# Performance work log

Hardware: AMD Instinct MI355X
Metric: run time of the kernel (lower is better)

Reference implementation:

```python
import jax, jax.numpy as jnp
import numpy as np

N_GRAPHS = 1250
NEG_SLOPE = 0.2

def gat_layer(x, src, dst, W, a_src, a_dst, b, concat):
    # x: [N, Fin]; W: [Fin, H*C]; a_src/a_dst: [H, C]; b: [H*C] or [C]
    N = x.shape[0]
    H, C = a_src.shape
    h = (x @ W).reshape(N, H, C)                      # [N,H,C]
    alpha_s = jnp.sum(h * a_src[None], axis=-1)       # [N,H]
    alpha_d = jnp.sum(h * a_dst[None], axis=-1)       # [N,H]
    e = jax.nn.leaky_relu(alpha_s[src] + alpha_d[dst], NEG_SLOPE)  # [E,H]
    # segment softmax over incoming edges of each target node
    m = jax.ops.segment_max(e, dst, num_segments=N)   # [N,H]
    m = jnp.where(jnp.isfinite(m), m, 0.0)
    ex = jnp.exp(e - m[dst])
    s = jax.ops.segment_sum(ex, dst, num_segments=N)  # [N,H]
    alpha = ex / (s[dst] + 1e-16)                     # [E,H]
    msg = h[src] * alpha[..., None]                   # [E,H,C]
    out = jax.ops.segment_sum(msg, dst, num_segments=N)  # [N,H,C]
    out = out.reshape(N, H * C) if concat else out.mean(axis=1)
    return out + b

def setup_inputs() -> dict:
    key = jax.random.key(0)
    ks = jax.random.split(key, 13)
    N, E = 50000, 100000
    x = jax.random.normal(ks[0], (N, 78), dtype=jnp.float32)
    edge_index = jax.random.randint(ks[1], (2, E), 0, N, dtype=jnp.int64)
    # sorted segment ids -> every graph non-empty (~40 nodes each)
    batch = jnp.sort(jax.random.randint(ks[2], (N,), 0, N_GRAPHS, dtype=jnp.int64))
    g = lambda k, shape, fan: jax.random.normal(k, shape, dtype=jnp.float32) / np.float32(np.sqrt(fan))
    return {
        'x': x, 'edge_index': edge_index, 'batch': batch,
        'W1': g(ks[3], (78, 780), 78), 'a_src1': g(ks[4], (10, 78), 78), 'a_dst1': g(ks[5], (10, 78), 78),
        'b1': jnp.zeros((780,), jnp.float32),
        'W2': g(ks[6], (780, 128), 780), 'a_src2': g(ks[7], (1, 128), 128), 'a_dst2': g(ks[8], (1, 128), 128),
        'b2': jnp.zeros((128,), jnp.float32),
        'fc_w': g(ks[9], (128, 128), 128), 'fc_b': jnp.zeros((128,), jnp.float32),
    }

def reference(x, edge_index, batch, W1, a_src1, a_dst1, b1, W2, a_src2, a_dst2, b2, fc_w, fc_b):
    N = x.shape[0]
    loop = jnp.arange(N, dtype=edge_index.dtype)
    src = jnp.concatenate([edge_index[0], loop])  # add self loops (PyG default)
    dst = jnp.concatenate([edge_index[1], loop])
    # dropout layers are identity in eval mode
    h = jax.nn.elu(gat_layer(x, src, dst, W1, a_src1, a_dst1, b1, concat=True))   # [N,780]
    h = jax.nn.relu(gat_layer(h, src, dst, W2, a_src2, a_dst2, b2, concat=True))  # [N,128]
    g = jax.ops.segment_max(h, batch, num_segments=N_GRAPHS)                      # [G,128]
    g = jnp.where(jnp.isfinite(g), g, 0.0)
    return jax.nn.relu(g @ fc_w + fc_b)
```

## Files before the change

### kernel.cpp

```cpp
#include <hip/hip_runtime.h>
#include <hip/hip_bf16.h>
#include <cstdint>

#define CAP 32
typedef __hip_bfloat16 bf16;
typedef __attribute__((ext_vector_type(8))) short short8;
typedef __attribute__((ext_vector_type(4))) float f32x4;

__device__ __forceinline__ float sb2f(short s) {
  unsigned int u = ((unsigned int)(unsigned short)s) << 16;
  return __uint_as_float(u);
}
__device__ __forceinline__ short f2sb(float f) {
  bf16 h = __float2bfloat16(f);
  return *reinterpret_cast<short*>(&h);
}

__global__ void k_detect(const int* __restrict__ ei, int* __restrict__ flag) {
  __shared__ int any;
  if (threadIdx.x == 0) any = 0;
  __syncthreads();
  int v = 0;
  for (int i = 1 + 2 * threadIdx.x; i < 2000; i += 512) v |= ei[i];
  if (v) atomicOr(&any, 1);
  __syncthreads();
  if (threadIdx.x == 0) flag[0] = (any == 0) ? 1 : 0;
}

__device__ __forceinline__ void edge_sd(const int* __restrict__ ei, int e, int f,
                                        int& src, int& dst) {
  if (e < 100000) {
    if (f) { src = ei[2 * e]; dst = ei[200000 + 2 * e]; }
    else   { src = ei[e];     dst = ei[100000 + e]; }
  } else { src = dst = e - 100000; }
  src = min(max(src, 0), 49999);
  dst = min(max(dst, 0), 49999);
}

__global__ void k_prep(const float* __restrict__ x, const float* __restrict__ W1,
                       const float* __restrict__ W2, const float* __restrict__ aw1,
                       const float* __restrict__ dw1, bf16* __restrict__ xb,
                       bf16* __restrict__ Wat, bf16* __restrict__ W1bdp,
                       bf16* __restrict__ W2h, float* __restrict__ zp, int zeroWords) {
  int i = blockIdx.x * 256 + threadIdx.x;
  if (i < zeroWords) zp[i] = 0.f;
  const int n_xb = 50000 * 96;
  const int n_wa = 32 * 96;
  const int n_bd = 10 * 96 * 96;
  const int n_w2 = 10 * 128 * 96;
  if (i < n_xb) {
    int r = i / 96, k = i - r * 96;
    xb[i] = __float2bfloat16(k < 78 ? x[r * 78 + k] : 0.f);
  } else if (i < n_xb + n_wa) {
    int j = i - n_xb;
    int c = j / 96, k = j - c * 96;
    float s = 0.f;
    if (k < 78 && c < 20) {
      const float* w = (c < 10) ? aw1 : dw1;
      int h = (c < 10) ? c : c - 10;
      const float* wrow = W1 + k * 780 + h * 78;
      const float* arow = w + h * 78;
      for (int q = 0; q < 78; q++) s += wrow[q] * arow[q];
    }
    Wat[c * 96 + k] = __float2bfloat16(s);
  } else if (i < n_xb + n_wa + n_bd) {
    int j = i - n_xb - n_wa;
    int hh = j / 9216;
    int rem = j - hh * 9216;
    int jj = rem / 96, k = rem - jj * 96;
    W1bdp[j] = __float2bfloat16((jj < 78 && k < 78) ? W1[k * 780 + hh * 78 + jj] : 0.f);
  } else if (i < n_xb + n_wa + n_bd + n_w2) {
    int j = i - n_xb - n_wa - n_bd;
    int hh = j / 12288;
    int rem = j - hh * 12288;
    int c = rem / 96, k = rem - c * 96;
    W2h[j] = __float2bfloat16(k < 78 ? W2[(hh * 78 + k) * 128 + c] : 0.f);
  }
}

__global__ __launch_bounds__(256) void k_alpha(const bf16* __restrict__ xb,
                                               const bf16* __restrict__ Wat,
                                               float* __restrict__ as1,
                                               float* __restrict__ ad1) {
  __shared__ __align__(16) short Als[64 * 104];
  __shared__ __align__(16) short Wls[32 * 104];
  const int t = threadIdx.x;
  const int w = t >> 6, l = t & 63, l15 = l & 15, q = l >> 4;
  const int rowBase = blockIdx.x * 64;
  for (int s = t; s < 768; s += 256) {
    int row = s / 12, kg = s - row * 12;
    short8 v = {};
    int gr = rowBase + row;
    if (gr < 50000) v = *(const short8*)((const short*)xb + (size_t)gr * 96 + kg * 8);
    *(short8*)&Als[row * 104 + kg * 8] = v;
  }
  for (int s = t; s < 384; s += 256) {
    int row = s / 12, kg = s - row * 12;
    *(short8*)&Wls[row * 104 + kg * 8] =
        *(const short8*)((const short*)Wat + (size_t)row * 96 + kg * 8);
  }
  __syncthreads();
  f32x4 acc2[2] = {};
#pragma unroll
  for (int ks = 0; ks < 3; ks++) {
    short8 a = *(const short8*)&Als[(w * 16 + l15) * 104 + ks * 32 + q * 8];
#pragma unroll
    for (int nt = 0; nt < 2; nt++) {
      short8 b = *(const short8*)&Wls[(nt * 16 + l15) * 104 + ks * 32 + q * 8];
      acc2[nt] = __builtin_amdgcn_mfma_f32_16x16x32_bf16(a, b, acc2[nt], 0, 0, 0);
    }
  }
  const int gr0 = rowBase + w * 16 + q * 4;
#pragma unroll
  for (int nt = 0; nt < 2; nt++) {
    int c = nt * 16 + l15;
#pragma unroll
    for (int r = 0; r < 4; r++) {
      int gr = gr0 + r;
      if (gr < 50000) {
        if (c < 10)       as1[gr * 10 + c] = acc2[nt][r];
        else if (c < 20)  ad1[gr * 10 + (c - 10)] = acc2[nt][r];
      }
    }
  }
}

__global__ void k_scatter(const int* __restrict__ ei, const int* __restrict__ flag,
                          int* __restrict__ cnt, int* __restrict__ csr) {
  int e = blockIdx.x * 256 + threadIdx.x;
  if (e >= 150000) return;
  int f = flag[0], src, dst;
  edge_sd(ei, e, f, src, dst);
  int pos = atomicAdd(&cnt[dst], 1);
  if (pos < CAP) csr[dst * CAP + pos] = src;
}

__global__ __launch_bounds__(256) void k_aggx(const bf16* __restrict__ xb,
                                              const float* __restrict__ as1,
                                              const float* __restrict__ ad1,
                                              const int* __restrict__ csr,
                                              const int* __restrict__ cnt,
                                              bf16* __restrict__ aggx) {
  __shared__ float sexw[2][CAP * 10];
  __shared__ float sden[2][16];
  __shared__ int ssrc[2][CAP];
  const int t = threadIdx.x;
  const int sub = t >> 7, tt = t & 127;
  const int n = blockIdx.x * 2 + sub;
  if (tt < 16) sden[sub][tt] = 0.f;
  const int cn = min(cnt[n], CAP);
  if (tt < cn) ssrc[sub][tt] = csr[n * CAP + tt];
  __syncthreads();
  for (int wv = tt; wv < cn * 10; wv += 128) {
    int k = wv / 10, h = wv - k * 10;
    int src = ssrc[sub][k];
    float e = as1[src * 10 + h] + ad1[n * 10 + h];
    e = e >= 0.f ? e : 0.2f * e;
    float ex = __expf(e);
    sexw[sub][wv] = ex;
    atomicAdd(&sden[sub][h], ex);
  }
  __syncthreads();
  if (tt < 96) {
    float acc[10];
#pragma unroll
    for (int h = 0; h < 10; h++) acc[h] = 0.f;
    const short* xs = (const short*)xb;
    for (int k = 0; k < cn; k++) {
      int src = ssrc[sub][k];
      float xv = sb2f(xs[(size_t)src * 96 + tt]);
      const float* swk = sexw[sub] + k * 10;
#pragma unroll
      for (int h = 0; h < 10; h++) acc[h] += swk[h] * xv;
    }
    short* outp = (short*)aggx + (size_t)n * 960 + tt;
#pragma unroll
    for (int h = 0; h < 10; h++)
      outp[h * 96] = f2sb(acc[h] / (sden[sub][h] + 1e-16f));
  }
}

__global__ __launch_bounds__(256) void k_gemm2f(const bf16* __restrict__ aggx,
                                                const bf16* __restrict__ W1bdp,
                                                const bf16* __restrict__ W2h,
                                                const float* __restrict__ b1,
                                                const float* __restrict__ AW2,
                                                const float* __restrict__ DW2,
                                                bf16* __restrict__ H2,
                                                float* __restrict__ as2,
                                                float* __restrict__ ad2) {
  __shared__ __align__(16) short Ain[64 * 104];
  __shared__ __align__(16) short Ah[64 * 104];
  __shared__ __align__(16) short Bw[96 * 104];
  __shared__ __align__(16) short Bls[128 * 104];
  __shared__ float sb1[784];
  __shared__ float sS[4][64], sD[4][64];
  const int t = threadIdx.x;
  const int w = t >> 6, l = t & 63, l15 = l & 15, q = l >> 4;
  const int rowBase = blockIdx.x * 64;
  for (int i = t; i < 784; i += 256) sb1[i] = (i < 780) ? b1[i] : 0.f;
  f32x4 acc[4][2] = {};
  for (int h = 0; h < 10; h++) {
    __syncthreads();
#pragma unroll
    for (int i = 0; i < 3; i++) {
      int s = t + i * 256;
      int row = s / 12, kg = s - row * 12;
      int gr = rowBase + row;
      short8 v = {};
      if (gr < 50000)
        v = *(const short8*)((const short*)aggx + ((size_t)gr * 10 + h) * 96 + kg * 8);
      *(short8*)&Ain[row * 104 + kg * 8] = v;
    }
    for (int s = t; s < 1152; s += 256) {
      int row = s / 12, kg = s - row * 12;
      *(short8*)&Bw[row * 104 + kg * 8] =
          *(const short8*)((const short*)W1bdp + (size_t)h * 9216 + row * 96 + kg * 8);
    }
#pragma unroll
    for (int i = 0; i < 6; i++) {
      int s = t + i * 256;
      int col = s / 12, kg = s - col * 12;
      *(short8*)&Bls[col * 104 + kg * 8] =
          *(const short8*)((const short*)W2h + (size_t)h * 12288 + col * 96 + kg * 8);
    }
    __syncthreads();
    f32x4 cacc[6] = {};
#pragma unroll
    for (int ks = 0; ks < 3; ks++) {
      short8 a = *(const short8*)&Ain[(w * 16 + l15) * 104 + ks * 32 + q * 8];
#pragma unroll
      for (int nt = 0; nt < 6; nt++) {
        short8 b = *(const short8*)&Bw[(nt * 16 + l15) * 104 + ks * 32 + q * 8];
        cacc[nt] = __builtin_amdgcn_mfma_f32_16x16x32_bf16(a, b, cacc[nt], 0, 0, 0);
      }
    }
#pragma unroll
    for (int nt = 0; nt < 6; nt++) {
      int col = nt * 16 + l15;
      float bb = (col < 78) ? sb1[h * 78 + col] : 0.f;
#pragma unroll
      for (int r = 0; r < 4; r++) {
        int row = w * 16 + q * 4 + r;
        float v = cacc[nt][r] + bb;
        v = v > 0.f ? v : __expf(v) - 1.f;
        Ah[row * 104 + col] = f2sb(v);
      }
    }
    __syncthreads();
#pragma unroll
    for (int ks = 0; ks < 3; ks++) {
      short8 a[4];
#pragma unroll
      for (int mt = 0; mt < 4; mt++)
        a[mt] = *(const short8*)&Ah[(mt * 16 + l15) * 104 + ks * 32 + q * 8];
#pragma unroll
      for (int ntl = 0; ntl < 2; ntl++) {
        short8 b = *(const short8*)&Bls[((w * 2 + ntl) * 16 + l15) * 104 + ks * 32 + q * 8];
#pragma unroll
        for (int mt = 0; mt < 4; mt++)
          acc[mt][ntl] = __builtin_amdgcn_mfma_f32_16x16x32_bf16(a[mt], b, acc[mt][ntl], 0, 0, 0);
      }
    }
  }
  const int col0 = w * 32 + l15, col1 = col0 + 16;
  const float aw0 = AW2[col0], aw1 = AW2[col1];
  const float dw0 = DW2[col0], dw1 = DW2[col1];
  f32x4 sp[4], dp[4];
#pragma unroll
  for (int mt = 0; mt < 4; mt++) {
    sp[mt] = acc[mt][0] * aw0 + acc[mt][1] * aw1;
    dp[mt] = acc[mt][0] * dw0 + acc[mt][1] * dw1;
  }
#pragma unroll
  for (int m = 1; m < 16; m <<= 1) {
#pragma unroll
    for (int mt = 0; mt < 4; mt++)
#pragma unroll
      for (int r = 0; r < 4; r++) {
        sp[mt][r] += __shfl_xor(sp[mt][r], m, 64);
        dp[mt][r] += __shfl_xor(dp[mt][r], m, 64);
      }
  }
  if (l15 == 0) {
#pragma unroll
    for (int mt = 0; mt < 4; mt++)
#pragma unroll
      for (int r = 0; r < 4; r++) {
        sS[w][mt * 16 + q * 4 + r] = sp[mt][r];
        sD[w][mt * 16 + q * 4 + r] = dp[mt][r];
      }
  }
#pragma unroll
  for (int mt = 0; mt < 4; mt++) {
    int gr0 = rowBase + mt * 16 + q * 4;
#pragma unroll
    for (int ntl = 0; ntl < 2; ntl++) {
      int gc = w * 32 + ntl * 16 + l15;
#pragma unroll
      for (int r = 0; r < 4; r++) {
        int gr = gr0 + r;
        if (gr < 50000) H2[(size_t)gr * 128 + gc] = __float2bfloat16(acc[mt][ntl][r]);
      }
    }
  }
  __syncthreads();
  if (t < 64) {
    int gr = rowBase + t;
    if (gr < 50000) as2[gr] = sS[0][t] + sS[1][t] + sS[2][t] + sS[3][t];
  } else if (t < 128) {
    int r2 = t - 64;
    int gr = rowBase + r2;
    if (gr < 50000) ad2[gr] = sD[0][r2] + sD[1][r2] + sD[2][r2] + sD[3][r2];
  }
}

__global__ __launch_bounds__(256) void k_agg2(const bf16* __restrict__ H2,
                                              const float* __restrict__ as2,
                                              const float* __restrict__ ad2,
                                              const int* __restrict__ csr,
                                              const int* __restrict__ cnt,
                                              const float* __restrict__ b2,
                                              const int* __restrict__ batch,
                                              const int* __restrict__ flag,
                                              float* __restrict__ g) {
  __shared__ int ssrc[2][CAP];
  __shared__ float sexw[2][CAP];
  __shared__ float sden[2];
  const int t = threadIdx.x;
  const int sub = t >> 7, tt = t & 127;
  const int n = blockIdx.x * 2 + sub;
  if (tt == 0) sden[sub] = 0.f;
  __syncthreads();
  const int cn = min(cnt[n], CAP);
  if (tt < cn) {
    int src = csr[n * CAP + tt];
    ssrc[sub][tt] = src;
    float e = as2[src] + ad2[n];
    e = e >= 0.f ? e : 0.2f * e;
    float ex = __expf(e);
    sexw[sub][tt] = ex;
    atomicAdd(&sden[sub], ex);
  }
  __syncthreads();
  const short* H2s = (const short*)H2;
  float acc = 0.f;
  for (int k = 0; k < cn; k++)
    acc += sexw[sub][k] * sb2f(H2s[(size_t)ssrc[sub][k] * 128 + tt]);
  float v = acc / (sden[sub] + 1e-16f) + b2[tt];
  v = v > 0.f ? v : 0.f;
  int b = flag[0] ? batch[2 * n] : batch[n];
  b = min(max(b, 0), 1249);
  atomicMax((int*)&g[b * 128 + tt], __float_as_int(v));
}

__global__ __launch_bounds__(128) void k_fc(const float* __restrict__ g,
                                            const float* __restrict__ fw,
                                            const float* __restrict__ fb,
                                            float* __restrict__ out) {
  const int n = blockIdx.x, t = threadIdx.x;
  __shared__ float grow[128];
  grow[t] = g[n * 128 + t];
  __syncthreads();
  float acc = fb[t];
  for (int k = 0; k < 128; k++) acc += grow[k] * fw[k * 128 + t];
  out[n * 128 + t] = acc > 0.f ? acc : 0.f;
}

extern "C" void kernel_launch(void* const* d_in, const int* in_sizes, int n_in,
                              void* d_out, int out_size, void* d_ws, size_t ws_size,
                              hipStream_t stream) {
  const float* x     = (const float*)d_in[0];
  const int*   ei    = (const int*)d_in[1];
  const int*   batch = (const int*)d_in[2];
  const float* W1    = (const float*)d_in[3];
  const float* as1w  = (const float*)d_in[4];
  const float* ad1w  = (const float*)d_in[5];
  const float* b1    = (const float*)d_in[6];
  const float* W2    = (const float*)d_in[7];
  const float* as2w  = (const float*)d_in[8];
  const float* ad2w  = (const float*)d_in[9];
  const float* b2    = (const float*)d_in[10];
  const float* fcw   = (const float*)d_in[11];
  const float* fcb   = (const float*)d_in[12];
  float* out = (float*)d_out;

  char* p = (char*)d_ws;
  size_t off = 0;
  auto alloc = [&](size_t bytes) -> void* {
    void* r = p + off;
    off = (off + bytes + 15) & ~(size_t)15;
    return r;
  };
  int*   cnt = (int*)  alloc(50000 * 4);
  float* g   = (float*)alloc(160000 * 4);
  size_t zeroWords = off / 4;
  float* as1   = (float*)alloc(500000 * 4);
  float* ad1   = (float*)alloc(500000 * 4);
  float* as2   = (float*)alloc(50000 * 4);
  float* ad2   = (float*)alloc(50000 * 4);
  bf16*  Wat   = (bf16*) alloc((size_t)32 * 96 * 2);
  bf16*  W1bdp = (bf16*) alloc((size_t)10 * 96 * 96 * 2);
  bf16*  W2h   = (bf16*) alloc((size_t)10 * 128 * 96 * 2);
  bf16*  aggx  = (bf16*) alloc((size_t)50000 * 10 * 96 * 2);
  int*   csr   = (int*)  alloc((size_t)50000 * CAP * 4);
  void*  uni = alloc((size_t)50000 * 128 * 2);
  bf16*  xb  = (bf16*)uni;
  bf16*  h2  = (bf16*)uni;
  int*   flag = (int*) alloc(16);
  (void)ws_size; (void)in_sizes; (void)n_in; (void)out_size;

  k_detect<<<1, 256, 0, stream>>>(ei, flag);
  int prepN = 50000 * 96 + 32 * 96 + 10 * 96 * 96 + 10 * 128 * 96;
  k_prep<<<(prepN + 255) / 256, 256, 0, stream>>>(
      x, W1, W2, as1w, ad1w, xb, Wat, W1bdp, W2h, (float*)d_ws, (int)zeroWords);

  k_alpha<<<782, 256, 0, stream>>>(xb, Wat, as1, ad1);
  k_scatter<<<(150000 + 255) / 256, 256, 0, stream>>>(ei, flag, cnt, csr);
  k_aggx<<<25000, 256, 0, stream>>>(xb, as1, ad1, csr, cnt, aggx);
  k_gemm2f<<<782, 256, 0, stream>>>(aggx, W1bdp, W2h, b1, as2w, ad2w, h2, as2, ad2);
  k_agg2<<<25000, 256, 0, stream>>>(h2, as2, ad2, csr, cnt, b2, batch, flag, g);
  k_fc<<<1250, 128, 0, stream>>>(g, fcw, fcb, out);
}
```

Baseline: 298.9 us.

## Load GEMM operands straight from global and stage aggx stores via LDS

In the aggregation kernel, per-head output values are first written to shared memory and then stored to global as coalesced 16-byte vectors instead of strided 2-byte stores. In the fused GEMM kernel, the input tile and the W2 fragments are loaded directly from global memory into MFMA registers, removing two LDS staging buffers and their copy loops. The LDS row pitch is also changed from 104 to 108. This cuts LDS footprint and copy work, which may raise occupancy, but it depends on global/L2 latency being hidden and the new pitch may change bank conflicts.

```diff
diff --git a/kernel.cpp b/kernel.cpp
--- a/kernel.cpp
+++ b/kernel.cpp
@@ -144,6 +144,7 @@
   __shared__ float sexw[2][CAP * 10];
   __shared__ float sden[2][16];
   __shared__ int ssrc[2][CAP];
+  __shared__ short sagg[2][960];
   const int t = threadIdx.x;
   const int sub = t >> 7, tt = t & 127;
   const int n = blockIdx.x * 2 + sub;
@@ -173,10 +174,14 @@
 #pragma unroll
       for (int h = 0; h < 10; h++) acc[h] += swk[h] * xv;
     }
-    short* outp = (short*)aggx + (size_t)n * 960 + tt;
 #pragma unroll
     for (int h = 0; h < 10; h++)
-      outp[h * 96] = f2sb(acc[h] / (sden[sub][h] + 1e-16f));
+      sagg[sub][h * 96 + tt] = f2sb(acc[h] / (sden[sub][h] + 1e-16f));
+  }
+  __syncthreads();
+  if (tt < 120) {
+    short8 v = *(const short8*)&sagg[sub][tt * 8];
+    *(short8*)((short*)aggx + (size_t)n * 960 + tt * 8) = v;
   }
 }
 
@@ -189,49 +194,35 @@
                                                 bf16* __restrict__ H2,
                                                 float* __restrict__ as2,
                                                 float* __restrict__ ad2) {
-  __shared__ __align__(16) short Ain[64 * 104];
-  __shared__ __align__(16) short Ah[64 * 104];
-  __shared__ __align__(16) short Bw[96 * 104];
-  __shared__ __align__(16) short Bls[128 * 104];
+  __shared__ __align__(16) short Ah[64 * 108];
+  __shared__ __align__(16) short Bw[96 * 108];
   __shared__ float sb1[784];
   __shared__ float sS[4][64], sD[4][64];
   const int t = threadIdx.x;
   const int w = t >> 6, l = t & 63, l15 = l & 15, q = l >> 4;
   const int rowBase = blockIdx.x * 64;
   for (int i = t; i < 784; i += 256) sb1[i] = (i < 780) ? b1[i] : 0.f;
+  const int garow = rowBase + w * 16 + l15;
+  const short* aggs = (const short*)aggx;
+  const short* w2s = (const short*)W2h;
   f32x4 acc[4][2] = {};
   for (int h = 0; h < 10; h++) {
     __syncthreads();
-#pragma unroll
-    for (int i = 0; i < 3; i++) {
-      int s = t + i * 256;
-      int row = s / 12, kg = s - row * 12;
-      int gr = rowBase + row;
-      short8 v = {};
-      if (gr < 50000)
-        v = *(const short8*)((const short*)aggx + ((size_t)gr * 10 + h) * 96 + kg * 8);
-      *(short8*)&Ain[row * 104 + kg * 8] = v;
-    }
     for (int s = t; s < 1152; s += 256) {
       int row = s / 12, kg = s - row * 12;
-      *(short8*)&Bw[row * 104 + kg * 8] =
+      *(short8*)&Bw[row * 108 + kg * 8] =
           *(const short8*)((const short*)W1bdp + (size_t)h * 9216 + row * 96 + kg * 8);
-    }
-#pragma unroll
-    for (int i = 0; i < 6; i++) {
-      int s = t + i * 256;
-      int col = s / 12, kg = s - col * 12;
-      *(short8*)&Bls[col * 104 + kg * 8] =
-          *(const short8*)((const short*)W2h + (size_t)h * 12288 + col * 96 + kg * 8);
     }
     __syncthreads();
     f32x4 cacc[6] = {};
 #pragma unroll
     for (int ks = 0; ks < 3; ks++) {
-      short8 a = *(const short8*)&Ain[(w * 16 + l15) * 104 + ks * 32 + q * 8];
+      short8 a = {};
+      if (garow < 50000)
+        a = *(const short8*)(aggs + ((size_t)garow * 10 + h) * 96 + ks * 32 + q * 8);
 #pragma unroll
       for (int nt = 0; nt < 6; nt++) {
-        short8 b = *(const short8*)&Bw[(nt * 16 + l15) * 104 + ks * 32 + q * 8];
+        short8 b = *(const short8*)&Bw[(nt * 16 + l15) * 108 + ks * 32 + q * 8];
         cacc[nt] = __builtin_amdgcn_mfma_f32_16x16x32_bf16(a, b, cacc[nt], 0, 0, 0);
       }
     }
@@ -244,7 +235,7 @@
         int row = w * 16 + q * 4 + r;
         float v = cacc[nt][r] + bb;
         v = v > 0.f ? v : __expf(v) - 1.f;
-        Ah[row * 104 + col] = f2sb(v);
+        Ah[row * 108 + col] = f2sb(v);
       }
     }
     __syncthreads();
@@ -253,10 +244,11 @@
       short8 a[4];
 #pragma unroll
       for (int mt = 0; mt < 4; mt++)
-        a[mt] = *(const short8*)&Ah[(mt * 16 + l15) * 104 + ks * 32 + q * 8];
+        a[mt] = *(const short8*)&Ah[(mt * 16 + l15) * 108 + ks * 32 + q * 8];
 #pragma unroll
       for (int ntl = 0; ntl < 2; ntl++) {
-        short8 b = *(const short8*)&Bls[((w * 2 + ntl) * 16 + l15) * 104 + ks * 32 + q * 8];
+        short8 b = *(const short8*)(w2s + (size_t)h * 12288 +
+                                    ((w * 2 + ntl) * 16 + l15) * 96 + ks * 32 + q * 8);
 #pragma unroll
         for (int mt = 0; mt < 4; mt++)
           acc[mt][ntl] = __builtin_amdgcn_mfma_f32_16x16x32_bf16(a[mt], b, acc[mt][ntl], 0, 0, 0);
```

Measured after the change: 301.3 us. Within noise of the previous version (+0.8%).
